# Optimization experiments

Measured on AMD Instinct MI355X. Metric: run time of the kernel, lower is better.

The kernel has to match this reference:

```python
import jax, jax.numpy as jnp
import numpy as np

N = 100_000
E = 1_600_000
IN, HID, OUT, ED = 128, 128, 64, 16
NEG_SLOPE = 0.2  # PyG GATConv default leaky_relu slope


def segment_softmax(logits, seg, num_segments):
    m = jax.ops.segment_max(logits, seg, num_segments=num_segments)
    m = jnp.where(jnp.isfinite(m), m, 0.0)
    e = jnp.exp(logits - m[seg])
    s = jax.ops.segment_sum(e, seg, num_segments=num_segments)
    return e / (s[seg] + 1e-16)


def gat_conv(x, edge_index, W, a_src, a_dst, b, edge_attr=None, We=None, ae=None):
    """PyG GATConv, heads=1, add_self_loops=True, fill_value='mean'."""
    n = x.shape[0]
    h = x @ W  # [N, C]
    loop = jnp.arange(n, dtype=edge_index.dtype)
    src = jnp.concatenate([edge_index[0], loop])  # [E+N]
    dst = jnp.concatenate([edge_index[1], loop])
    alpha = (h * a_src).sum(-1)[src] + (h * a_dst).sum(-1)[dst]  # [E+N]
    if edge_attr is not None:
        # self-loop edge_attr filled with per-destination mean (PyG fill_value='mean')
        cnt = jax.ops.segment_sum(jnp.ones((edge_attr.shape[0],), edge_attr.dtype), edge_index[1], num_segments=n)
        mean_attr = jax.ops.segment_sum(edge_attr, edge_index[1], num_segments=n) / jnp.maximum(cnt, 1.0)[:, None]
        ea = jnp.concatenate([edge_attr, mean_attr], axis=0)  # [E+N, ED]
        alpha = alpha + (ea @ We) @ ae
    alpha = jax.nn.leaky_relu(alpha, NEG_SLOPE)
    alpha = segment_softmax(alpha, dst, n)
    out = jax.ops.segment_sum(alpha[:, None] * h[src], dst, num_segments=n)  # scatter-add
    return out + b


def setup_inputs() -> dict:
    key = jax.random.key(0)
    ks = iter(jax.random.split(key, 32))
    g = lambda shape, fan: (jax.random.normal(next(ks), shape, jnp.float32) * (1.0 / np.sqrt(fan)))
    inp = {
        "x": jax.random.normal(next(ks), (N, IN), jnp.float32),
        "edge_index": jax.random.randint(next(ks), (2, E), 0, N, jnp.int32),
        "edge_attr": jax.random.normal(next(ks), (E, ED), jnp.float32),
        # conv1 (no edge_attr)
        "W1": g((IN, HID), IN), "a1_src": g((HID,), HID), "a1_dst": g((HID,), HID), "b1": jnp.zeros((HID,), jnp.float32),
        # conv2 (with edge_attr)
        "W2": g((HID, HID), HID), "a2_src": g((HID,), HID), "a2_dst": g((HID,), HID), "b2": jnp.zeros((HID,), jnp.float32),
        "We2": g((ED, HID), ED), "ae2": g((HID,), HID),
        # initial residual linear
        "Wr": g((IN, HID), IN), "br": jnp.zeros((HID,), jnp.float32),
        # conv_mu
        "Wmu": g((HID, OUT), HID), "amu_src": g((OUT,), OUT), "amu_dst": g((OUT,), OUT), "bmu": jnp.zeros((OUT,), jnp.float32),
        "Wemu": g((ED, OUT), ED), "aemu": g((OUT,), OUT),
        # conv_logstd
        "Wls": g((HID, OUT), HID), "als_src": g((OUT,), OUT), "als_dst": g((OUT,), OUT), "bls": jnp.zeros((OUT,), jnp.float32),
        "Wels": g((ED, OUT), ED), "aels": g((OUT,), OUT),
    }
    return inp


def reference(x, edge_index, edge_attr,
              W1, a1_src, a1_dst, b1,
              W2, a2_src, a2_dst, b2, We2, ae2,
              Wr, br,
              Wmu, amu_src, amu_dst, bmu, Wemu, aemu,
              Wls, als_src, als_dst, bls, Wels, aels):
    h = jax.nn.relu(gat_conv(x, edge_index, W1, a1_src, a1_dst, b1))
    h = jax.nn.relu(gat_conv(h, edge_index, W2, a2_src, a2_dst, b2, edge_attr, We2, ae2))
    h = h + (x @ Wr + br)  # initial residual
    mu = gat_conv(h, edge_index, Wmu, amu_src, amu_dst, bmu, edge_attr, Wemu, aemu)
    logstd = gat_conv(h, edge_index, Wls, als_src, als_dst, bls, edge_attr, Wels, aels)
    return mu, logstd
```

## Files before the change

### kernel.cpp

```cpp
#include <hip/hip_runtime.h>

#define NN 100000
#define NE 1600000
#define BSH 9
#define NBUK 196

typedef __attribute__((ext_vector_type(8))) short bf16x8;
typedef __attribute__((ext_vector_type(4))) float f32x4;

__device__ __forceinline__ float grp_sum16(float v){
  #pragma unroll
  for (int o = 8; o; o >>= 1) v += __shfl_xor(v, o, 16);
  return v;
}
__device__ __forceinline__ float grp_sum32(float v){
  #pragma unroll
  for (int o = 16; o; o >>= 1) v += __shfl_xor(v, o, 32);
  return v;
}
__device__ __forceinline__ float bf2f(unsigned short x){
  return __uint_as_float(((unsigned)x) << 16);
}
__device__ __forceinline__ unsigned short f2bf(float f){
  unsigned u = __float_as_uint(f);
  return (unsigned short)((u + 0x7FFFu + ((u >> 16) & 1u)) >> 16);
}

__global__ void prep_w_kernel(const float* __restrict__ W1, const float* __restrict__ W2,
                              const float* __restrict__ Wr, const float* __restrict__ Wmu,
                              const float* __restrict__ Wls,
                              unsigned short* __restrict__ W1t, unsigned short* __restrict__ W2t,
                              unsigned short* __restrict__ Wrt, unsigned short* __restrict__ Wmlt){
  int b = blockIdx.x, t = threadIdx.x;
  for (int it = 0; it < 64; it++){
    int idx = it*256 + t;
    int k = idx >> 7, c = idx & 127;
    float v; unsigned short* dst;
    if (b == 0){ v = W1[k*128+c]; dst = W1t; }
    else if (b == 1){ v = W2[k*128+c]; dst = W2t; }
    else if (b == 2){ v = Wr[k*128+c]; dst = Wrt; }
    else { v = (c & 1) ? Wls[k*64 + (c>>1)] : Wmu[k*64 + (c>>1)]; dst = Wmlt; }
    dst[c*128 + k] = f2bf(v);
  }
}

__global__ void wvec_kernel(const float* __restrict__ We2, const float* __restrict__ ae2,
                            const float* __restrict__ Wemu, const float* __restrict__ aemu,
                            const float* __restrict__ Wels, const float* __restrict__ aels,
                            float* __restrict__ wv){
  int t = threadIdx.x;
  if (t < 16){
    float s = 0.f; for (int c = 0; c < 128; c++) s += We2[t*128+c]*ae2[c];
    wv[t] = s;
  } else if (t < 32){
    int k = t-16; float s = 0.f; for (int c = 0; c < 64; c++) s += Wemu[k*64+c]*aemu[c];
    wv[16+k] = s;
  } else if (t < 48){
    int k = t-32; float s = 0.f; for (int c = 0; c < 64; c++) s += Wels[k*64+c]*aels[c];
    wv[32+k] = s;
  }
}

__global__ void cast_x_kernel(const float* __restrict__ x, unsigned short* __restrict__ Xb){
  int i = blockIdx.x*256 + threadIdx.x;
  if (i >= NN*128/8) return;
  const float4* src = (const float4*)x + (size_t)i*2;
  float4 v0 = src[0], v1 = src[1];
  ushort4 o0 = make_ushort4(f2bf(v0.x), f2bf(v0.y), f2bf(v0.z), f2bf(v0.w));
  ushort4 o1 = make_ushort4(f2bf(v1.x), f2bf(v1.y), f2bf(v1.z), f2bf(v1.w));
  *(ushort4*)(Xb + (size_t)i*8)     = o0;
  *(ushort4*)(Xb + (size_t)i*8 + 4) = o1;
}

__global__ void zero_kernel(int* __restrict__ p, int n){
  int i = blockIdx.x*256 + threadIdx.x;
  if (i < n) p[i] = 0;
}

__global__ __launch_bounds__(1024) void ehist_kernel(const int* __restrict__ ei,
                                                     unsigned* __restrict__ gbcnt){
  __shared__ unsigned h[256];
  int t = threadIdx.x;
  if (t < 256) h[t] = 0;
  __syncthreads();
  int e0 = blockIdx.x*4096 + t;
  #pragma unroll
  for (int k = 0; k < 4; k++){
    int e = e0 + k*1024;
    if (e < NE) atomicAdd(&h[ei[NE+e] >> BSH], 1);
  }
  __syncthreads();
  if (t < 256 && h[t]) atomicAdd(&gbcnt[t], h[t]);
}

__global__ void bscan_kernel(const unsigned* __restrict__ gbcnt,
                             unsigned* __restrict__ gbbase, int* __restrict__ rowptr){
  __shared__ unsigned sh[256];
  int t = threadIdx.x;
  unsigned v = gbcnt[t];
  sh[t] = v; __syncthreads();
  for (int o = 1; o < 256; o <<= 1){
    unsigned add = (t >= o) ? sh[t-o] : 0;
    __syncthreads();
    sh[t] += add;
    __syncthreads();
  }
  gbbase[t+1] = sh[t];
  if (t == 0){ gbbase[0] = 0; rowptr[NN] = NE; }
}

__global__ __launch_bounds__(1024) void bin_kernel(const int* __restrict__ ei,
                                                   const float* __restrict__ ea,
                                                   const float* __restrict__ wv,
                                                   const unsigned* __restrict__ gbbase,
                                                   unsigned* __restrict__ gbfill,
                                                   uint2* __restrict__ bdu,
                                                   float4* __restrict__ bw){
  __shared__ unsigned hcnt[256], hbase[256], hcur[256];
  __shared__ float wvs[48];
  int t = threadIdx.x;
  if (t < 256){ hcnt[t] = 0; hcur[t] = 0; }
  else if (t >= 256 && t < 304) wvs[t-256] = wv[t-256];
  __syncthreads();
  int d[4], u[4], b[4]; float4 w[4]; bool val[4];
  int e0 = blockIdx.x*4096 + t;
  #pragma unroll
  for (int k = 0; k < 4; k++){
    int e = e0 + k*1024;
    val[k] = e < NE;
    if (val[k]){
      d[k] = ei[NE+e]; u[k] = ei[e];
      b[k] = d[k] >> BSH;
      atomicAdd(&hcnt[b[k]], 1);
      const float4* p = (const float4*)(ea + (size_t)e*16);
      float a[16]; float4 vv;
      vv = p[0]; a[0]=vv.x; a[1]=vv.y; a[2]=vv.z; a[3]=vv.w;
      vv = p[1]; a[4]=vv.x; a[5]=vv.y; a[6]=vv.z; a[7]=vv.w;
      vv = p[2]; a[8]=vv.x; a[9]=vv.y; a[10]=vv.z; a[11]=vv.w;
      vv = p[3]; a[12]=vv.x; a[13]=vv.y; a[14]=vv.z; a[15]=vv.w;
      float s2 = 0.f, smu = 0.f, sls = 0.f;
      #pragma unroll
      for (int q = 0; q < 16; q++){
        s2  = fmaf(a[q], wvs[q],    s2);
        smu = fmaf(a[q], wvs[16+q], smu);
        sls = fmaf(a[q], wvs[32+q], sls);
      }
      w[k] = make_float4(s2, smu, sls, 0.f);
    }
  }
  __syncthreads();
  if (t < 256){
    unsigned c = hcnt[t];
    hbase[t] = c ? atomicAdd(&gbfill[t], c) : 0u;
  }
  __syncthreads();
  #pragma unroll
  for (int k = 0; k < 4; k++){
    if (val[k]){
      unsigned pos = atomicAdd(&hcur[b[k]], 1);
      unsigned slot = gbbase[b[k]] + hbase[b[k]] + pos;
      bdu[slot] = make_uint2((unsigned)d[k], (unsigned)u[k]);
      bw[slot]  = w[k];
    }
  }
}

__global__ __launch_bounds__(1024) void place_kernel(const uint2* __restrict__ bdu,
                                                     const float4* __restrict__ bw,
                                                     const unsigned* __restrict__ gbbase,
                                                     int* __restrict__ rowptr,
                                                     unsigned* __restrict__ csr_u,
                                                     float* __restrict__ ewp2,
                                                     float2* __restrict__ ewpmuls){
  __shared__ unsigned h[512], incl[512], cur[512];
  int b = blockIdx.x, t = threadIdx.x;
  unsigned cbase = gbbase[b];
  unsigned cnt = gbbase[b+1] - cbase;
  if (t < 512) h[t] = 0;
  __syncthreads();
  for (unsigned i = t; i < cnt; i += 1024)
    atomicAdd(&h[bdu[cbase+i].x & 511], 1);
  __syncthreads();
  if (t < 512) incl[t] = h[t];
  __syncthreads();
  for (int o = 1; o < 512; o <<= 1){
    unsigned add = (t >= o && t < 512) ? incl[t-o] : 0;
    __syncthreads();
    if (t < 512) incl[t] += add;
    __syncthreads();
  }
  if (t < 512){
    cur[t] = 0;
    int node = (b << BSH) + t;
    if (node < NN) rowptr[node] = (int)(cbase + incl[t] - h[t]);
  }
  __syncthreads();
  for (unsigned i = t; i < cnt; i += 1024){
    uint2 du = bdu[cbase+i];
    unsigned ld = du.x & 511;
    unsigned pos = atomicAdd(&cur[ld], 1);
    unsigned slot = cbase + (incl[ld] - h[ld]) + pos;
    float4 w = bw[cbase+i];
    csr_u[slot] = du.y;
    ewp2[slot] = w.x;
    ewpmuls[slot] = make_float2(w.y, w.z);
  }
}

template<bool OUTF32, int DOTS>
__global__ __launch_bounds__(256) void gemm_bf16(const unsigned short* __restrict__ Xb,
                                                 const unsigned short* __restrict__ Wt,
                                                 void* __restrict__ Y,
                                                 const float* __restrict__ bias, int nrows,
                                                 const float* __restrict__ va,
                                                 const float* __restrict__ vb,
                                                 const float* __restrict__ vc,
                                                 const float* __restrict__ vd,
                                                 float* __restrict__ sOut,
                                                 float* __restrict__ dOut){
  __shared__ uint4 As[128*16];
  __shared__ uint4 Bs[128*16];
  int t = threadIdx.x;
  int row0 = blockIdx.x * 128;
  #pragma unroll
  for (int p = 0; p < 8; p++){
    int idx = p*256 + t;
    int r = idx >> 4, cir = idx & 15;
    uint4 v = make_uint4(0,0,0,0);
    if (row0 + r < nrows) v = *(const uint4*)(Xb + ((size_t)(row0+r))*128 + cir*8);
    As[r*16 + (cir ^ (r & 7))] = v;
  }
  #pragma unroll
  for (int p = 0; p < 8; p++){
    int idx = p*256 + t;
    int r = idx >> 4, cir = idx & 15;
    Bs[r*16 + (cir ^ (r & 7))] = *(const uint4*)(Wt + (size_t)r*128 + cir*8);
  }
  __syncthreads();
  int w = t >> 6, l = t & 63;
  int lr = l & 15;
  int lk = l >> 4;
  const bf16x8* As8 = (const bf16x8*)As;
  const bf16x8* Bs8 = (const bf16x8*)Bs;
  f32x4 acc[2][8];
  f32x4 zero = {0.f, 0.f, 0.f, 0.f};
  #pragma unroll
  for (int m = 0; m < 2; m++)
    #pragma unroll
    for (int n = 0; n < 8; n++) acc[m][n] = zero;
  #pragma unroll
  for (int ks = 0; ks < 4; ks++){
    bf16x8 a0, a1, bf[8];
    { int r = w*32 + lr;      a0 = As8[r*16 + ((ks*4+lk) ^ (r&7))]; }
    { int r = w*32 + 16 + lr; a1 = As8[r*16 + ((ks*4+lk) ^ (r&7))]; }
    #pragma unroll
    for (int nt = 0; nt < 8; nt++){
      int r = nt*16 + lr;
      bf[nt] = Bs8[r*16 + ((ks*4+lk) ^ (r&7))];
    }
    #pragma unroll
    for (int nt = 0; nt < 8; nt++){
      acc[0][nt] = __builtin_amdgcn_mfma_f32_16x16x32_bf16(a0, bf[nt], acc[0][nt], 0, 0, 0);
      acc[1][nt] = __builtin_amdgcn_mfma_f32_16x16x32_bf16(a1, bf[nt], acc[1][nt], 0, 0, 0);
    }
  }
  if constexpr (DOTS == 1){
    #pragma unroll
    for (int mt = 0; mt < 2; mt++){
      #pragma unroll
      for (int i = 0; i < 4; i++){
        float ps = 0.f, pd = 0.f;
        #pragma unroll
        for (int nt = 0; nt < 8; nt++){
          float av = acc[mt][nt][i];
          int col = nt*16 + lr;
          ps = fmaf(av, va[col], ps);
          pd = fmaf(av, vb[col], pd);
        }
        ps = grp_sum16(ps); pd = grp_sum16(pd);
        int r = row0 + w*32 + mt*16 + lk*4 + i;
        if (lr == 0 && r < nrows){ sOut[r] = ps; dOut[r] = pd; }
      }
    }
  }
  if constexpr (DOTS == 2){
    #pragma unroll
    for (int mt = 0; mt < 2; mt++){
      #pragma unroll
      for (int i = 0; i < 4; i++){
        float pmu = 0.f, pdm = 0.f, pls = 0.f, pdl = 0.f;
        #pragma unroll
        for (int nt = 0; nt < 8; nt++){
          float av = acc[mt][nt][i];
          int col = nt*16 + lr;
          int c = col >> 1;
          if (col & 1){ pls = fmaf(av, vc[c], pls); pdl = fmaf(av, vd[c], pdl); }
          else        { pmu = fmaf(av, va[c], pmu); pdm = fmaf(av, vb[c], pdm); }
        }
        pmu = grp_sum16(pmu); pdm = grp_sum16(pdm);
        pls = grp_sum16(pls); pdl = grp_sum16(pdl);
        int r = row0 + w*32 + mt*16 + lk*4 + i;
        if (lr == 0 && r < nrows){
          ((float2*)sOut)[r] = make_float2(pmu, pls);
          ((float2*)dOut)[r] = make_float2(pdm, pdl);
        }
      }
    }
  }
  #pragma unroll
  for (int mt = 0; mt < 2; mt++){
    int gr0 = row0 + w*32 + mt*16 + lk*4;
    #pragma unroll
    for (int nt = 0; nt < 8; nt++){
      int col = nt*16 + lr;
      float bv = OUTF32 ? bias[col] : 0.f;
      #pragma unroll
      for (int i = 0; i < 4; i++){
        int r = gr0 + i;
        if (r < nrows){
          float o = acc[mt][nt][i];
          if constexpr (OUTF32) ((float*)Y)[(size_t)r*128 + col] = o + bv;
          else ((unsigned short*)Y)[(size_t)r*128 + col] = f2bf(o);
        }
      }
    }
  }
}

template<bool HAS_EW>
__global__ __launch_bounds__(256) void agg_conv(const unsigned short* __restrict__ Hb,
                                                const float* __restrict__ s,
                                                const float* __restrict__ dsc,
                                                const float* __restrict__ ewp,
                                                const int* __restrict__ rowptr,
                                                const unsigned* __restrict__ csr_u,
                                                const float* __restrict__ bias,
                                                const float* __restrict__ resid,
                                                unsigned short* __restrict__ out){
  int v = (blockIdx.x * blockDim.x + threadIdx.x) >> 5;
  int lig = threadIdx.x & 31;
  if (v >= NN) return;
  int rs = rowptr[v], re = rowptr[v+1];
  int deg = re - rs;
  float d_v = dsc[v];
  float acc[4] = {0.f,0.f,0.f,0.f};
  float pl = 0.f, ewl = 0.f;
  for (int base = rs; base < re; base += 32){
    int i = base + lig;
    int u = 0; float w = 0.f;
    if (i < re){
      u = (int)csr_u[i];
      float e = HAS_EW ? ewp[i] : 0.f;
      if (HAS_EW) ewl += e;
      float a = s[u] + d_v + e;
      float l = a > 0.f ? a : 0.2f*a;
      w = __expf(l);
    }
    pl += w;
    int nv = re - base; if (nv > 32) nv = 32;
    for (int j = 0; j < nv; j += 8){
      uint2 q[8]; float wj[8];
      #pragma unroll
      for (int k = 0; k < 8; k++){
        int uk = __shfl(u, j+k, 32);
        wj[k] = __shfl(w, j+k, 32);
        q[k] = *(const uint2*)(Hb + (size_t)uk*128 + lig*4);
      }
      #pragma unroll
      for (int k = 0; k < 8; k++){
        acc[0] = fmaf(wj[k], __uint_as_float(q[k].x << 16), acc[0]);
        acc[1] = fmaf(wj[k], __uint_as_float(q[k].x & 0xFFFF0000u), acc[1]);
        acc[2] = fmaf(wj[k], __uint_as_float(q[k].y << 16), acc[2]);
        acc[3] = fmaf(wj[k], __uint_as_float(q[k].y & 0xFFFF0000u), acc[3]);
      }
    }
  }
  float p = grp_sum32(pl);
  float ews = HAS_EW ? grp_sum32(ewl) : 0.f;
  float selfa = s[v] + d_v + (HAS_EW ? ews / (float)(deg > 1 ? deg : 1) : 0.f);
  float lself = selfa > 0.f ? selfa : 0.2f*selfa;
  float wself = __expf(lself);
  p += wself;
  {
    uint2 q = *(const uint2*)(Hb + (size_t)v*128 + lig*4);
    acc[0] = fmaf(wself, __uint_as_float(q.x << 16), acc[0]);
    acc[1] = fmaf(wself, __uint_as_float(q.x & 0xFFFF0000u), acc[1]);
    acc[2] = fmaf(wself, __uint_as_float(q.y << 16), acc[2]);
    acc[3] = fmaf(wself, __uint_as_float(q.y & 0xFFFF0000u), acc[3]);
  }
  float inv = 1.f / p;
  int c0 = lig*4;
  float4 bv = *(const float4*)(bias + c0);
  float o0 = fmaxf(acc[0]*inv + bv.x, 0.f);
  float o1 = fmaxf(acc[1]*inv + bv.y, 0.f);
  float o2 = fmaxf(acc[2]*inv + bv.z, 0.f);
  float o3 = fmaxf(acc[3]*inv + bv.w, 0.f);
  if (HAS_EW){
    float4 r0 = *(const float4*)(resid + (size_t)v*128 + c0);
    o0 += r0.x; o1 += r0.y; o2 += r0.z; o3 += r0.w;
  }
  uint2 ow;
  ow.x = (unsigned)f2bf(o0) | ((unsigned)f2bf(o1) << 16);
  ow.y = (unsigned)f2bf(o2) | ((unsigned)f2bf(o3) << 16);
  *(uint2*)(out + (size_t)v*128 + c0) = ow;
}

__global__ __launch_bounds__(256) void agg_muls(const unsigned short* __restrict__ Yb,
                                                const float2* __restrict__ sg,
                                                const float2* __restrict__ dg,
                                                const float2* __restrict__ ewpmuls,
                                                const int* __restrict__ rowptr,
                                                const unsigned* __restrict__ csr_u,
                                                const float* __restrict__ bmu,
                                                const float* __restrict__ bls,
                                                float* __restrict__ outmu,
                                                float* __restrict__ outls){
  int v = (blockIdx.x * blockDim.x + threadIdx.x) >> 5;
  int lig = threadIdx.x & 31;
  if (v >= NN) return;
  int rs = rowptr[v], re = rowptr[v+1];
  int deg = re - rs;
  float2 dv = dg[v];
  float accmu[2] = {0.f,0.f}, accls[2] = {0.f,0.f};
  float pmu = 0.f, pls = 0.f, ewlmu = 0.f, ewlls = 0.f;
  for (int base = rs; base < re; base += 32){
    int i = base + lig;
    int u = 0; float wmu = 0.f, wls = 0.f;
    if (i < re){
      u = (int)csr_u[i];
      float2 su = sg[u];
      float2 ee = ewpmuls[i];
      ewlmu += ee.x; ewlls += ee.y;
      float amu = su.x + dv.x + ee.x;
      float als = su.y + dv.y + ee.y;
      float lmu = amu > 0.f ? amu : 0.2f*amu;
      float lls = als > 0.f ? als : 0.2f*als;
      wmu = __expf(lmu); wls = __expf(lls);
    }
    pmu += wmu; pls += wls;
    int nv = re - base; if (nv > 32) nv = 32;
    for (int j = 0; j < nv; j += 8){
      uint2 q[8]; float wm[8], wl[8];
      #pragma unroll
      for (int k = 0; k < 8; k++){
        int uk = __shfl(u, j+k, 32);
        wm[k] = __shfl(wmu, j+k, 32);
        wl[k] = __shfl(wls, j+k, 32);
        q[k] = *(const uint2*)(Yb + (size_t)uk*128 + lig*4);
      }
      #pragma unroll
      for (int k = 0; k < 8; k++){
        accmu[0] = fmaf(wm[k], __uint_as_float(q[k].x << 16), accmu[0]);
        accls[0] = fmaf(wl[k], __uint_as_float(q[k].x & 0xFFFF0000u), accls[0]);
        accmu[1] = fmaf(wm[k], __uint_as_float(q[k].y << 16), accmu[1]);
        accls[1] = fmaf(wl[k], __uint_as_float(q[k].y & 0xFFFF0000u), accls[1]);
      }
    }
  }
  float Pmu = grp_sum32(pmu), Pls = grp_sum32(pls);
  float Emu = grp_sum32(ewlmu), Els = grp_sum32(ewlls);
  float2 sv = sg[v];
  float dnm = (float)(deg > 1 ? deg : 1);
  float selfmu = sv.x + dv.x + Emu/dnm;
  float selfls = sv.y + dv.y + Els/dnm;
  float lmu = selfmu > 0.f ? selfmu : 0.2f*selfmu;
  float lls = selfls > 0.f ? selfls : 0.2f*selfls;
  float wmu_s = __expf(lmu), wls_s = __expf(lls);
  Pmu += wmu_s; Pls += wls_s;
  {
    uint2 q = *(const uint2*)(Yb + (size_t)v*128 + lig*4);
    accmu[0] = fmaf(wmu_s, __uint_as_float(q.x << 16), accmu[0]);
    accls[0] = fmaf(wls_s, __uint_as_float(q.x & 0xFFFF0000u), accls[0]);
    accmu[1] = fmaf(wmu_s, __uint_as_float(q.y << 16), accmu[1]);
    accls[1] = fmaf(wls_s, __uint_as_float(q.y & 0xFFFF0000u), accls[1]);
  }
  float imu = 1.f/Pmu, ils = 1.f/Pls;
  int c0 = lig*2;
  float2 omu = make_float2(accmu[0]*imu + bmu[c0], accmu[1]*imu + bmu[c0+1]);
  float2 ols = make_float2(accls[0]*ils + bls[c0], accls[1]*ils + bls[c0+1]);
  *(float2*)(outmu + (size_t)v*64 + c0) = omu;
  *(float2*)(outls + (size_t)v*64 + c0) = ols;
}

extern "C" void kernel_launch(void* const* d_in, const int* in_sizes, int n_in,
                              void* d_out, int out_size, void* d_ws, size_t ws_size,
                              hipStream_t stream){
  const float* x    = (const float*)d_in[0];
  const int*   ei   = (const int*)  d_in[1];
  const float* ea   = (const float*)d_in[2];
  const float* W1   = (const float*)d_in[3];
  const float* a1s  = (const float*)d_in[4];
  const float* a1d  = (const float*)d_in[5];
  const float* b1   = (const float*)d_in[6];
  const float* W2   = (const float*)d_in[7];
  const float* a2s  = (const float*)d_in[8];
  const float* a2d  = (const float*)d_in[9];
  const float* b2   = (const float*)d_in[10];
  const float* We2  = (const float*)d_in[11];
  const float* ae2  = (const float*)d_in[12];
  const float* Wr   = (const float*)d_in[13];
  const float* br   = (const float*)d_in[14];
  const float* Wmu  = (const float*)d_in[15];
  const float* amus = (const float*)d_in[16];
  const float* amud = (const float*)d_in[17];
  const float* bmu  = (const float*)d_in[18];
  const float* Wemu = (const float*)d_in[19];
  const float* aemu = (const float*)d_in[20];
  const float* Wls  = (const float*)d_in[21];
  const float* alss = (const float*)d_in[22];
  const float* alsd = (const float*)d_in[23];
  const float* bls  = (const float*)d_in[24];
  const float* Wels = (const float*)d_in[25];
  const float* aels = (const float*)d_in[26];

  char* base = (char*)d_ws;
  size_t off = 0;
  auto alloc = [&](size_t bytes)->char*{
    char* p = base + off;
    off = (off + bytes + 511) & ~(size_t)511;
    return p;
  };
  int*      rowptr = (int*)   alloc((size_t)(NN+1)*4);
  unsigned* gbcnt  = (unsigned*)alloc(512*4);
  unsigned* gbfill = gbcnt + 256;
  unsigned* gbbase = (unsigned*)alloc(257*4);
  uint2*    bdu    = (uint2*) alloc((size_t)NE*8);
  float4*   bw     = (float4*)alloc((size_t)NE*16);
  unsigned* csr_u  = (unsigned*)alloc((size_t)NE*4);
  float*    ewp2   = (float*) alloc((size_t)NE*4);
  float2*   ewpmls = (float2*)alloc((size_t)NE*8);
  float*    wv     = (float*) alloc(48*4);
  float*    s1     = (float*) alloc((size_t)NN*4);
  float*    d1     = (float*) alloc((size_t)NN*4);
  float2*   sg2    = (float2*)alloc((size_t)NN*8);
  float2*   dg2    = (float2*)alloc((size_t)NN*8);
  unsigned short* W1t  = (unsigned short*)alloc(128*128*2);
  unsigned short* W2t  = (unsigned short*)alloc(128*128*2);
  unsigned short* Wrt  = (unsigned short*)alloc(128*128*2);
  unsigned short* Wmlt = (unsigned short*)alloc(128*128*2);
  unsigned short* Xb   = (unsigned short*)alloc((size_t)NN*128*2);
  unsigned short* bufA = (unsigned short*)alloc((size_t)NN*128*2);
  unsigned short* bufB = (unsigned short*)alloc((size_t)NN*128*2);
  if (off > ws_size) return;

  float* outF = (float*)d_out;
  float* muO  = outF;
  float* lsO  = outF + (size_t)NN*64;

  const int HB   = (NE + 4095)/4096;
  const int WB32 = (NN*32 + 255)/256;
  const int GB   = (NN + 127)/128;
  const int CB   = (NN*128/8 + 255)/256;

  prep_w_kernel<<<4, 256, 0, stream>>>(W1, W2, Wr, Wmu, Wls, W1t, W2t, Wrt, Wmlt);
  wvec_kernel<<<1, 64, 0, stream>>>(We2, ae2, Wemu, aemu, Wels, aels, wv);
  cast_x_kernel<<<CB, 256, 0, stream>>>(x, Xb);
  zero_kernel<<<2, 256, 0, stream>>>((int*)gbcnt, 512);
  ehist_kernel<<<HB, 1024, 0, stream>>>(ei, gbcnt);
  bscan_kernel<<<1, 256, 0, stream>>>(gbcnt, gbbase, rowptr);
  bin_kernel<<<HB, 1024, 0, stream>>>(ei, ea, wv, gbbase, gbfill, bdu, bw);
  place_kernel<<<NBUK, 1024, 0, stream>>>(bdu, bw, gbbase, rowptr, csr_u, ewp2, ewpmls);

  gemm_bf16<false,1><<<GB, 256, 0, stream>>>(Xb, W1t, bufA, nullptr, NN,
                                             a1s, a1d, nullptr, nullptr, s1, d1);
  agg_conv<false><<<WB32, 256, 0, stream>>>(bufA, s1, d1, nullptr, rowptr, csr_u,
                                            b1, nullptr, bufB);
  gemm_bf16<false,1><<<GB, 256, 0, stream>>>(bufB, W2t, bufA, nullptr, NN,
                                             a2s, a2d, nullptr, nullptr, s1, d1);
  gemm_bf16<true,0><<<GB, 256, 0, stream>>>(Xb, Wrt, outF, br, NN,
                                            nullptr, nullptr, nullptr, nullptr,
                                            nullptr, nullptr);
  agg_conv<true><<<WB32, 256, 0, stream>>>(bufA, s1, d1, ewp2, rowptr, csr_u,
                                           b2, outF, bufB);
  gemm_bf16<false,2><<<GB, 256, 0, stream>>>(bufB, Wmlt, bufA, nullptr, NN,
                                             amus, amud, alss, alsd,
                                             (float*)sg2, (float*)dg2);
  agg_muls<<<WB32, 256, 0, stream>>>(bufA, sg2, dg2, ewpmls, rowptr, csr_u,
                                     bmu, bls, muO, lsO);
}
```

Baseline: 453.1 us.

## Process several nodes per warp-group in aggregation and store residual as bf16

The aggregation kernels now let each 32-lane group loop over 8 consecutive destination nodes instead of one, with bias loads hoisted out of the loop. The grid shrinks eightfold, which cuts launch and per-group setup overhead. The residual projection x@Wr+br is now written as bf16 to a new buffer rather than fp32 into the output, halving its write and read traffic. The risks are less parallelism to hide gather latency, imbalance from degree variation within each 8-node chunk, and slightly lower residual precision.

New measurement: 491.6 us. +8.5%, slower.

```diff
diff --git a/kernel.cpp b/kernel.cpp
--- a/kernel.cpp
+++ b/kernel.cpp
@@ -4,6 +4,7 @@
 #define NE 1600000
 #define BSH 9
 #define NBUK 196
+#define NPG 8
 
 typedef __attribute__((ext_vector_type(8))) short bf16x8;
 typedef __attribute__((ext_vector_type(4))) float f32x4;
@@ -207,7 +208,7 @@
   }
 }
 
-template<bool OUTF32, int DOTS>
+template<int OUT, int DOTS>
 __global__ __launch_bounds__(256) void gemm_bf16(const unsigned short* __restrict__ Xb,
                                                  const unsigned short* __restrict__ Wt,
                                                  void* __restrict__ Y,
@@ -313,13 +314,13 @@
     #pragma unroll
     for (int nt = 0; nt < 8; nt++){
       int col = nt*16 + lr;
-      float bv = OUTF32 ? bias[col] : 0.f;
+      float bv = (OUT >= 1) ? bias[col] : 0.f;
       #pragma unroll
       for (int i = 0; i < 4; i++){
         int r = gr0 + i;
         if (r < nrows){
-          float o = acc[mt][nt][i];
-          if constexpr (OUTF32) ((float*)Y)[(size_t)r*128 + col] = o + bv;
+          float o = acc[mt][nt][i] + bv;
+          if constexpr (OUT == 1) ((float*)Y)[(size_t)r*128 + col] = o;
           else ((unsigned short*)Y)[(size_t)r*128 + col] = f2bf(o);
         }
       }
@@ -335,74 +336,80 @@
                                                 const int* __restrict__ rowptr,
                                                 const unsigned* __restrict__ csr_u,
                                                 const float* __restrict__ bias,
-                                                const float* __restrict__ resid,
+                                                const unsigned short* __restrict__ residb,
                                                 unsigned short* __restrict__ out){
-  int v = (blockIdx.x * blockDim.x + threadIdx.x) >> 5;
+  int g = (blockIdx.x * blockDim.x + threadIdx.x) >> 5;
   int lig = threadIdx.x & 31;
-  if (v >= NN) return;
-  int rs = rowptr[v], re = rowptr[v+1];
-  int deg = re - rs;
-  float d_v = dsc[v];
-  float acc[4] = {0.f,0.f,0.f,0.f};
-  float pl = 0.f, ewl = 0.f;
-  for (int base = rs; base < re; base += 32){
-    int i = base + lig;
-    int u = 0; float w = 0.f;
-    if (i < re){
-      u = (int)csr_u[i];
-      float e = HAS_EW ? ewp[i] : 0.f;
-      if (HAS_EW) ewl += e;
-      float a = s[u] + d_v + e;
-      float l = a > 0.f ? a : 0.2f*a;
-      w = __expf(l);
-    }
-    pl += w;
-    int nv = re - base; if (nv > 32) nv = 32;
-    for (int j = 0; j < nv; j += 8){
-      uint2 q[8]; float wj[8];
-      #pragma unroll
-      for (int k = 0; k < 8; k++){
-        int uk = __shfl(u, j+k, 32);
-        wj[k] = __shfl(w, j+k, 32);
-        q[k] = *(const uint2*)(Hb + (size_t)uk*128 + lig*4);
-      }
-      #pragma unroll
-      for (int k = 0; k < 8; k++){
-        acc[0] = fmaf(wj[k], __uint_as_float(q[k].x << 16), acc[0]);
-        acc[1] = fmaf(wj[k], __uint_as_float(q[k].x & 0xFFFF0000u), acc[1]);
-        acc[2] = fmaf(wj[k], __uint_as_float(q[k].y << 16), acc[2]);
-        acc[3] = fmaf(wj[k], __uint_as_float(q[k].y & 0xFFFF0000u), acc[3]);
-      }
-    }
-  }
-  float p = grp_sum32(pl);
-  float ews = HAS_EW ? grp_sum32(ewl) : 0.f;
-  float selfa = s[v] + d_v + (HAS_EW ? ews / (float)(deg > 1 ? deg : 1) : 0.f);
-  float lself = selfa > 0.f ? selfa : 0.2f*selfa;
-  float wself = __expf(lself);
-  p += wself;
-  {
-    uint2 q = *(const uint2*)(Hb + (size_t)v*128 + lig*4);
-    acc[0] = fmaf(wself, __uint_as_float(q.x << 16), acc[0]);
-    acc[1] = fmaf(wself, __uint_as_float(q.x & 0xFFFF0000u), acc[1]);
-    acc[2] = fmaf(wself, __uint_as_float(q.y << 16), acc[2]);
-    acc[3] = fmaf(wself, __uint_as_float(q.y & 0xFFFF0000u), acc[3]);
-  }
-  float inv = 1.f / p;
   int c0 = lig*4;
   float4 bv = *(const float4*)(bias + c0);
-  float o0 = fmaxf(acc[0]*inv + bv.x, 0.f);
-  float o1 = fmaxf(acc[1]*inv + bv.y, 0.f);
-  float o2 = fmaxf(acc[2]*inv + bv.z, 0.f);
-  float o3 = fmaxf(acc[3]*inv + bv.w, 0.f);
-  if (HAS_EW){
-    float4 r0 = *(const float4*)(resid + (size_t)v*128 + c0);
-    o0 += r0.x; o1 += r0.y; o2 += r0.z; o3 += r0.w;
-  }
-  uint2 ow;
-  ow.x = (unsigned)f2bf(o0) | ((unsigned)f2bf(o1) << 16);
-  ow.y = (unsigned)f2bf(o2) | ((unsigned)f2bf(o3) << 16);
-  *(uint2*)(out + (size_t)v*128 + c0) = ow;
+  int v0 = g * NPG;
+  int vend = v0 + NPG; if (vend > NN) vend = NN;
+  for (int v = v0; v < vend; v++){
+    int rs = rowptr[v], re = rowptr[v+1];
+    int deg = re - rs;
+    float d_v = dsc[v];
+    float acc[4] = {0.f,0.f,0.f,0.f};
+    float pl = 0.f, ewl = 0.f;
+    for (int base = rs; base < re; base += 32){
+      int i = base + lig;
+      int u = 0; float w = 0.f;
+      if (i < re){
+        u = (int)csr_u[i];
+        float e = HAS_EW ? ewp[i] : 0.f;
+        if (HAS_EW) ewl += e;
+        float a = s[u] + d_v + e;
+        float l = a > 0.f ? a : 0.2f*a;
+        w = __expf(l);
+      }
+      pl += w;
+      int nv = re - base; if (nv > 32) nv = 32;
+      for (int j = 0; j < nv; j += 8){
+        uint2 q[8]; float wj[8];
+        #pragma unroll
+        for (int k = 0; k < 8; k++){
+          int uk = __shfl(u, j+k, 32);
+          wj[k] = __shfl(w, j+k, 32);
+          q[k] = *(const uint2*)(Hb + (size_t)uk*128 + c0);
+        }
+        #pragma unroll
+        for (int k = 0; k < 8; k++){
+          acc[0] = fmaf(wj[k], __uint_as_float(q[k].x << 16), acc[0]);
+          acc[1] = fmaf(wj[k], __uint_as_float(q[k].x & 0xFFFF0000u), acc[1]);
+          acc[2] = fmaf(wj[k], __uint_as_float(q[k].y << 16), acc[2]);
+          acc[3] = fmaf(wj[k], __uint_as_float(q[k].y & 0xFFFF0000u), acc[3]);
+        }
+      }
+    }
+    float p = grp_sum32(pl);
+    float ews = HAS_EW ? grp_sum32(ewl) : 0.f;
+    float selfa = s[v] + d_v + (HAS_EW ? ews / (float)(deg > 1 ? deg : 1) : 0.f);
+    float lself = selfa > 0.f ? selfa : 0.2f*selfa;
+    float wself = __expf(lself);
+    p += wself;
+    {
+      uint2 q = *(const uint2*)(Hb + (size_t)v*128 + c0);
+      acc[0] = fmaf(wself, __uint_as_float(q.x << 16), acc[0]);
+      acc[1] = fmaf(wself, __uint_as_float(q.x & 0xFFFF0000u), acc[1]);
+      acc[2] = fmaf(wself, __uint_as_float(q.y << 16), acc[2]);
+      acc[3] = fmaf(wself, __uint_as_float(q.y & 0xFFFF0000u), acc[3]);
+    }
+    float inv = 1.f / p;
+    float o0 = fmaxf(acc[0]*inv + bv.x, 0.f);
+    float o1 = fmaxf(acc[1]*inv + bv.y, 0.f);
+    float o2 = fmaxf(acc[2]*inv + bv.z, 0.f);
+    float o3 = fmaxf(acc[3]*inv + bv.w, 0.f);
+    if (HAS_EW){
+      uint2 r = *(const uint2*)(residb + (size_t)v*128 + c0);
+      o0 += __uint_as_float(r.x << 16);
+      o1 += __uint_as_float(r.x & 0xFFFF0000u);
+      o2 += __uint_as_float(r.y << 16);
+      o3 += __uint_as_float(r.y & 0xFFFF0000u);
+    }
+    uint2 ow;
+    ow.x = (unsigned)f2bf(o0) | ((unsigned)f2bf(o1) << 16);
+    ow.y = (unsigned)f2bf(o2) | ((unsigned)f2bf(o3) << 16);
+    *(uint2*)(out + (size_t)v*128 + c0) = ow;
+  }
 }
 
 __global__ __launch_bounds__(256) void agg_muls(const unsigned short* __restrict__ Yb,
@@ -415,71 +422,76 @@
                                                 const float* __restrict__ bls,
                                                 float* __restrict__ outmu,
                                                 float* __restrict__ outls){
-  int v = (blockIdx.x * blockDim.x + threadIdx.x) >> 5;
+  int g = (blockIdx.x * blockDim.x + threadIdx.x) >> 5;
   int lig = threadIdx.x & 31;
-  if (v >= NN) return;
-  int rs = rowptr[v], re = rowptr[v+1];
-  int deg = re - rs;
-  float2 dv = dg[v];
-  float accmu[2] = {0.f,0.f}, accls[2] = {0.f,0.f};
-  float pmu = 0.f, pls = 0.f, ewlmu = 0.f, ewlls = 0.f;
-  for (int base = rs; base < re; base += 32){
-    int i = base + lig;
-    int u = 0; float wmu = 0.f, wls = 0.f;
-    if (i < re){
-      u = (int)csr_u[i];
-      float2 su = sg[u];
-      float2 ee = ewpmuls[i];
-      ewlmu += ee.x; ewlls += ee.y;
-      float amu = su.x + dv.x + ee.x;
-      float als = su.y + dv.y + ee.y;
-      float lmu = amu > 0.f ? amu : 0.2f*amu;
-      float lls = als > 0.f ? als : 0.2f*als;
-      wmu = __expf(lmu); wls = __expf(lls);
-    }
-    pmu += wmu; pls += wls;
-    int nv = re - base; if (nv > 32) nv = 32;
-    for (int j = 0; j < nv; j += 8){
-      uint2 q[8]; float wm[8], wl[8];
-      #pragma unroll
-      for (int k = 0; k < 8; k++){
-        int uk = __shfl(u, j+k, 32);
-        wm[k] = __shfl(wmu, j+k, 32);
-        wl[k] = __shfl(wls, j+k, 32);
-        q[k] = *(const uint2*)(Yb + (size_t)uk*128 + lig*4);
-      }
-      #pragma unroll
-      for (int k = 0; k < 8; k++){
-        accmu[0] = fmaf(wm[k], __uint_as_float(q[k].x << 16), accmu[0]);
-        accls[0] = fmaf(wl[k], __uint_as_float(q[k].x & 0xFFFF0000u), accls[0]);
-        accmu[1] = fmaf(wm[k], __uint_as_float(q[k].y << 16), accmu[1]);
-        accls[1] = fmaf(wl[k], __uint_as_float(q[k].y & 0xFFFF0000u), accls[1]);
-      }
-    }
-  }
-  float Pmu = grp_sum32(pmu), Pls = grp_sum32(pls);
-  float Emu = grp_sum32(ewlmu), Els = grp_sum32(ewlls);
-  float2 sv = sg[v];
-  float dnm = (float)(deg > 1 ? deg : 1);
-  float selfmu = sv.x + dv.x + Emu/dnm;
-  float selfls = sv.y + dv.y + Els/dnm;
-  float lmu = selfmu > 0.f ? selfmu : 0.2f*selfmu;
-  float lls = selfls > 0.f ? selfls : 0.2f*selfls;
-  float wmu_s = __expf(lmu), wls_s = __expf(lls);
-  Pmu += wmu_s; Pls += wls_s;
-  {
-    uint2 q = *(const uint2*)(Yb + (size_t)v*128 + lig*4);
-    accmu[0] = fmaf(wmu_s, __uint_as_float(q.x << 16), accmu[0]);
-    accls[0] = fmaf(wls_s, __uint_as_float(q.x & 0xFFFF0000u), accls[0]);
-    accmu[1] = fmaf(wmu_s, __uint_as_float(q.y << 16), accmu[1]);
-    accls[1] = fmaf(wls_s, __uint_as_float(q.y & 0xFFFF0000u), accls[1]);
-  }
-  float imu = 1.f/Pmu, ils = 1.f/Pls;
   int c0 = lig*2;
-  float2 omu = make_float2(accmu[0]*imu + bmu[c0], accmu[1]*imu + bmu[c0+1]);
-  float2 ols = make_float2(accls[0]*ils + bls[c0], accls[1]*ils + bls[c0+1]);
-  *(float2*)(outmu + (size_t)v*64 + c0) = omu;
-  *(float2*)(outls + (size_t)v*64 + c0) = ols;
+  float2 bmv = make_float2(bmu[c0], bmu[c0+1]);
+  float2 blv = make_float2(bls[c0], bls[c0+1]);
+  int v0 = g * NPG;
+  int vend = v0 + NPG; if (vend > NN) vend = NN;
+  for (int v = v0; v < vend; v++){
+    int rs = rowptr[v], re = rowptr[v+1];
+    int deg = re - rs;
+    float2 dv = dg[v];
+    float accmu[2] = {0.f,0.f}, accls[2] = {0.f,0.f};
+    float pmu = 0.f, pls = 0.f, ewlmu = 0.f, ewlls = 0.f;
+    for (int base = rs; base < re; base += 32){
+      int i = base + lig;
+      int u = 0; float wmu = 0.f, wls = 0.f;
+      if (i < re){
+        u = (int)csr_u[i];
+        float2 su = sg[u];
+        float2 ee = ewpmuls[i];
+        ewlmu += ee.x; ewlls += ee.y;
+        float amu = su.x + dv.x + ee.x;
+        float als = su.y + dv.y + ee.y;
+        float lmu = amu > 0.f ? amu : 0.2f*amu;
+        float lls = als > 0.f ? als : 0.2f*als;
+        wmu = __expf(lmu); wls = __expf(lls);
+      }
+      pmu += wmu; pls += wls;
+      int nv = re - base; if (nv > 32) nv = 32;
+      for (int j = 0; j < nv; j += 8){
+        uint2 q[8]; float wm[8], wl[8];
+        #pragma unroll
+        for (int k = 0; k < 8; k++){
+          int uk = __shfl(u, j+k, 32);
+          wm[k] = __shfl(wmu, j+k, 32);
+          wl[k] = __shfl(wls, j+k, 32);
+          q[k] = *(const uint2*)(Yb + (size_t)uk*128 + lig*4);
+        }
+        #pragma unroll
+        for (int k = 0; k < 8; k++){
+          accmu[0] = fmaf(wm[k], __uint_as_float(q[k].x << 16), accmu[0]);
+          accls[0] = fmaf(wl[k], __uint_as_float(q[k].x & 0xFFFF0000u), accls[0]);
+          accmu[1] = fmaf(wm[k], __uint_as_float(q[k].y << 16), accmu[1]);
+          accls[1] = fmaf(wl[k], __uint_as_float(q[k].y & 0xFFFF0000u), accls[1]);
+        }
+      }
+    }
+    float Pmu = grp_sum32(pmu), Pls = grp_sum32(pls);
+    float Emu = grp_sum32(ewlmu), Els = grp_sum32(ewlls);
+    float2 sv = sg[v];
+    float dnm = (float)(deg > 1 ? deg : 1);
+    float selfmu = sv.x + dv.x + Emu/dnm;
+    float selfls = sv.y + dv.y + Els/dnm;
+    float lmu = selfmu > 0.f ? selfmu : 0.2f*selfmu;
+    float lls = selfls > 0.f ? selfls : 0.2f*selfls;
+    float wmu_s = __expf(lmu), wls_s = __expf(lls);
+    Pmu += wmu_s; Pls += wls_s;
+    {
+      uint2 q = *(const uint2*)(Yb + (size_t)v*128 + lig*4);
+      accmu[0] = fmaf(wmu_s, __uint_as_float(q.x << 16), accmu[0]);
+      accls[0] = fmaf(wls_s, __uint_as_float(q.x & 0xFFFF0000u), accls[0]);
+      accmu[1] = fmaf(wmu_s, __uint_as_float(q.y << 16), accmu[1]);
+      accls[1] = fmaf(wls_s, __uint_as_float(q.y & 0xFFFF0000u), accls[1]);
+    }
+    float imu = 1.f/Pmu, ils = 1.f/Pls;
+    float2 omu = make_float2(accmu[0]*imu + bmv.x, accmu[1]*imu + bmv.y);
+    float2 ols = make_float2(accls[0]*ils + blv.x, accls[1]*ils + blv.y);
+    *(float2*)(outmu + (size_t)v*64 + c0) = omu;
+    *(float2*)(outls + (size_t)v*64 + c0) = ols;
+  }
 }
 
 extern "C" void kernel_launch(void* const* d_in, const int* in_sizes, int n_in,
@@ -539,6 +551,7 @@
   unsigned short* Wrt  = (unsigned short*)alloc(128*128*2);
   unsigned short* Wmlt = (unsigned short*)alloc(128*128*2);
   unsigned short* Xb   = (unsigned short*)alloc((size_t)NN*128*2);
+  unsigned short* XRb  = (unsigned short*)alloc((size_t)NN*128*2);
   unsigned short* bufA = (unsigned short*)alloc((size_t)NN*128*2);
   unsigned short* bufB = (unsigned short*)alloc((size_t)NN*128*2);
   if (off > ws_size) return;
@@ -548,7 +561,7 @@
   float* lsO  = outF + (size_t)NN*64;
 
   const int HB   = (NE + 4095)/4096;
-  const int WB32 = (NN*32 + 255)/256;
+  const int AGB  = ((NN + NPG - 1)/NPG * 32 + 255)/256;
   const int GB   = (NN + 127)/128;
   const int CB   = (NN*128/8 + 255)/256;
 
@@ -561,20 +574,20 @@
   bin_kernel<<<HB, 1024, 0, stream>>>(ei, ea, wv, gbbase, gbfill, bdu, bw);
   place_kernel<<<NBUK, 1024, 0, stream>>>(bdu, bw, gbbase, rowptr, csr_u, ewp2, ewpmls);
 
-  gemm_bf16<false,1><<<GB, 256, 0, stream>>>(Xb, W1t, bufA, nullptr, NN,
-                                             a1s, a1d, nullptr, nullptr, s1, d1);
-  agg_conv<false><<<WB32, 256, 0, stream>>>(bufA, s1, d1, nullptr, rowptr, csr_u,
-                                            b1, nullptr, bufB);
-  gemm_bf16<false,1><<<GB, 256, 0, stream>>>(bufB, W2t, bufA, nullptr, NN,
-                                             a2s, a2d, nullptr, nullptr, s1, d1);
-  gemm_bf16<true,0><<<GB, 256, 0, stream>>>(Xb, Wrt, outF, br, NN,
-                                            nullptr, nullptr, nullptr, nullptr,
-                                            nullptr, nullptr);
-  agg_conv<true><<<WB32, 256, 0, stream>>>(bufA, s1, d1, ewp2, rowptr, csr_u,
-                                           b2, outF, bufB);
-  gemm_bf16<false,2><<<GB, 256, 0, stream>>>(bufB, Wmlt, bufA, nullptr, NN,
-                                             amus, amud, alss, alsd,
-                                             (float*)sg2, (float*)dg2);
-  agg_muls<<<WB32, 256, 0, stream>>>(bufA, sg2, dg2, ewpmls, rowptr, csr_u,
-                                     bmu, bls, muO, lsO);
-}
+  gemm_bf16<0,1><<<GB, 256, 0, stream>>>(Xb, W1t, bufA, nullptr, NN,
+                                         a1s, a1d, nullptr, nullptr, s1, d1);
+  agg_conv<false><<<AGB, 256, 0, stream>>>(bufA, s1, d1, nullptr, rowptr, csr_u,
+                                           b1, nullptr, bufB);
+  gemm_bf16<0,1><<<GB, 256, 0, stream>>>(bufB, W2t, bufA, nullptr, NN,
+                                         a2s, a2d, nullptr, nullptr, s1, d1);
+  gemm_bf16<2,0><<<GB, 256, 0, stream>>>(Xb, Wrt, XRb, br, NN,
+                                         nullptr, nullptr, nullptr, nullptr,
+                                         nullptr, nullptr);
+  agg_conv<true><<<AGB, 256, 0, stream>>>(bufA, s1, d1, ewp2, rowptr, csr_u,
+                                          b2, XRb, bufB);
+  gemm_bf16<0,2><<<GB, 256, 0, stream>>>(bufB, Wmlt, bufA, nullptr, NN,
+                                         amus, amud, alss, alsd,
+                                         (float*)sg2, (float*)dg2);
+  agg_muls<<<AGB, 256, 0, stream>>>(bufA, sg2, dg2, ewpmls, rowptr, csr_u,
+                                    bmu, bls, muO, lsO);
+}
```
